# Performance work log

Measured on AMD Instinct MI355X. Metric: run time of the kernel, lower is better.

## Reference

```python
import jax, jax.numpy as jnp
import numpy as np


def setup_inputs() -> dict:
    key = jax.random.key(0)
    k1, k2 = jax.random.split(key)
    n = 12000
    dataset = jax.random.normal(k1, (n,), dtype=jnp.float32)
    weights = jax.random.uniform(k2, (n,), dtype=jnp.float32)
    return {"dataset": dataset, "weights": weights}


def reference(dataset, weights):
    # normalize weights (update_weights)
    w = weights / jnp.sum(weights)
    neff = jnp.sum(w) ** 2 / jnp.sum(w ** 2)
    # Silverman's factor (torch.std is unbiased -> ddof=1; torch.quantile is linear interp)
    std_dev = jnp.std(dataset, ddof=1)
    iqr = jnp.quantile(dataset, 0.75) - jnp.quantile(dataset, 0.25)
    sigma_hat = jnp.minimum(std_dev, iqr / 1.34)
    h = 0.9 * sigma_hat * neff ** (-0.2)
    inv_norm = 1.0 / (h * jnp.sqrt(2.0 * jnp.pi))
    # pairwise Gaussian kernel matrix: [n, n]
    diff = (dataset[:, None] - dataset[None, :]) / h
    kernel = jnp.exp(-0.5 * diff * diff) * inv_norm
    pdf = kernel @ w  # [n]
    return jnp.log(pdf + 1e-10)
```

## Files before the change

### kernel.cpp

```cpp
#include <hip/hip_runtime.h>
#include <math.h>


#define BLK 256
#define NB 2048
#define NPART 12
#define CUT 4.0f

#if defined(__has_builtin)
#if __has_builtin(__builtin_amdgcn_exp2f)
#define EXP2(x) __builtin_amdgcn_exp2f(x)
#endif
#endif
#ifndef EXP2
#define EXP2(x) exp2f(x)
#endif

__global__ __launch_bounds__(1024) void kM(const float* __restrict__ d,
                                           const float* __restrict__ w,
                                           float4* __restrict__ statP,
                                           float2* __restrict__ mmP,
                                           float* __restrict__ gZero,
                                           int n) {
    __shared__ float4 sstat[16];
    __shared__ float2 smm[16];
    const int t = threadIdx.x, lane = t & 63, wid = t >> 6;
    if (t < 512) gZero[blockIdx.x * 512 + t] = 0.f;

    const int i = blockIdx.x * 1024 + t;
    const bool ok = (i < n);
    float dv = ok ? d[i] : 0.f;
    float wv = ok ? w[i] : 0.f;
    float mn = ok ? dv : __int_as_float(0x7f800000);
    float mx = ok ? dv : __int_as_float(0xff800000);
    float s1 = wv, s2 = wv * wv, sd = dv, sd2 = dv * dv;
    for (int off = 32; off > 0; off >>= 1) {
        s1 += __shfl_down(s1, off); s2 += __shfl_down(s2, off);
        sd += __shfl_down(sd, off); sd2 += __shfl_down(sd2, off);
        mn = fminf(mn, __shfl_down(mn, off));
        mx = fmaxf(mx, __shfl_down(mx, off));
    }
    if (lane == 0) { sstat[wid] = make_float4(s1, s2, sd, sd2); smm[wid] = make_float2(mn, mx); }
    __syncthreads();
    if (t == 0) {
        float4 a = sstat[0]; float2 m = smm[0];
        for (int q = 1; q < 16; ++q) {
            float4 b = sstat[q];
            a.x += b.x; a.y += b.y; a.z += b.z; a.w += b.w;
            m.x = fminf(m.x, smm[q].x); m.y = fmaxf(m.y, smm[q].y);
        }
        statP[blockIdx.x] = a;
        mmP[blockIdx.x] = m;
    }
}

__global__ __launch_bounds__(1024) void kA(const float* __restrict__ d,
                                           const float* __restrict__ w,
                                           const float2* __restrict__ mmP,
                                           int* __restrict__ gH,
                                           float* __restrict__ gW,
                                           float* __restrict__ gWE,
                                           int n) {
    __shared__ int   hl[NB];
    __shared__ float wl[NB];
    __shared__ float wel[NB];
    const int t = threadIdx.x;

    hl[t] = 0; hl[t + 1024] = 0;
    wl[t] = 0.f; wl[t + 1024] = 0.f;
    wel[t] = 0.f; wel[t + 1024] = 0.f;

    float lo = __int_as_float(0x7f800000), hi = __int_as_float(0xff800000);
    #pragma unroll
    for (int p = 0; p < NPART; ++p) {
        float2 m = mmP[p];
        lo = fminf(lo, m.x); hi = fmaxf(hi, m.y);
    }
    const float range = hi - lo;
    const float scale = (range > 0.f) ? (float)NB / range : 0.f;
    __syncthreads();

    const int i = blockIdx.x * 1024 + t;
    if (i < n) {
        float dv = d[i], wv = w[i];
        int b = (int)((dv - lo) * scale);
        b = b < NB ? b : NB - 1;
        atomicAdd(&hl[b], 1);
        atomicAdd(&wl[b], wv);
        atomicAdd(&wel[b], wv * dv);
    }
    __syncthreads();

    #pragma unroll
    for (int k = 0; k < 2; ++k) {
        int b = t + k * 1024;
        int hv = hl[b];
        if (hv) {
            atomicAdd(&gH[b], hv);
            atomicAdd(&gW[b], wl[b]);
            atomicAdd(&gWE[b], wel[b]);
        }
    }
}

__global__ __launch_bounds__(BLK) void k3(const float* __restrict__ d,
                                          const float4* __restrict__ statP,
                                          const float2* __restrict__ mmP,
                                          const int* __restrict__ gH,
                                          const float* __restrict__ gW,
                                          const float* __restrict__ gWE,
                                          float* __restrict__ out, int n) {
    __shared__ float2 sb[NB];
    __shared__ int cum[NB];
    __shared__ int woff[4];
    __shared__ int tbin[4], tprev[4];
    __shared__ float spar[4];
    __shared__ float sred[BLK];
    const int t = threadIdx.x, lane = t & 63, wv = t >> 6;

    float lo = __int_as_float(0x7f800000), hi = __int_as_float(0xff800000);
    #pragma unroll
    for (int p = 0; p < NPART; ++p) {
        float2 m = mmP[p];
        lo = fminf(lo, m.x); hi = fmaxf(hi, m.y);
    }
    const float range = hi - lo;
    const float scale = (range > 0.f) ? (float)NB / range : 0.f;
    const float binw = (scale > 0.f) ? 1.0f / scale : 0.f;

    const int base = t * 8;
    int h8[8], pre[8];
    int s = 0;
    #pragma unroll
    for (int k = 0; k < 8; ++k) {
        int b = base + k;
        h8[k] = gH[b];
        sb[b] = make_float2(gWE[b], gW[b]);
        s += h8[k];
        pre[k] = s;
    }
    int v = s;
    for (int off = 1; off < 64; off <<= 1) {
        int u = __shfl_up(v, off);
        if (lane >= off) v += u;
    }
    if (lane == 63) woff[wv] = v;
    __syncthreads();
    int wexcl = 0;
    #pragma unroll
    for (int q = 0; q < 4; ++q) if (q < wv) wexcl += woff[q];
    const int texcl = wexcl + (v - s);
    #pragma unroll
    for (int k = 0; k < 8; ++k) cum[base + k] = texcl + pre[k];

    const double p25 = 0.25 * (double)(n - 1);
    const double p75 = 0.75 * (double)(n - 1);
    const int l25 = (int)p25, l75 = (int)p75;
    const int u25 = (l25 + 1 < n) ? l25 + 1 : l25;
    const int u75 = (l75 + 1 < n) ? l75 + 1 : l75;
    const int targets[4] = {l25, u25, l75, u75};
    #pragma unroll
    for (int k = 0; k < 8; ++k) {
        int prev = texcl + (k ? pre[k - 1] : 0);
        int incl = texcl + pre[k];
        #pragma unroll
        for (int r = 0; r < 4; ++r)
            if (prev <= targets[r] && targets[r] < incl) { tbin[r] = base + k; tprev[r] = prev; }
    }
    __syncthreads();

    if (t == 0) {
        float qv[4];
        #pragma unroll
        for (int r = 0; r < 4; ++r) {
            int b = tbin[r];
            int cnt = cum[b] - tprev[r];
            float pos = (float)b + ((float)(targets[r] - tprev[r]) + 0.5f) / (float)cnt;
            qv[r] = lo + pos * binw;
        }
        double S1 = 0, S2 = 0, Sd = 0, Sd2 = 0;
        for (int p = 0; p < NPART; ++p) {
            float4 a = statP[p];
            S1 += a.x; S2 += a.y; Sd += a.z; Sd2 += a.w;
        }
        float neff = (float)(S1 * S1 / S2);
        float varf = (float)((Sd2 - Sd * Sd / (double)n) / ((double)n - 1.0));
        float sdev = sqrtf(varf);
        float f25 = (float)(p25 - (double)l25), f75 = (float)(p75 - (double)l75);
        float q25 = qv[0] + f25 * (qv[1] - qv[0]);
        float q75 = qv[2] + f75 * (qv[3] - qv[2]);
        float sig = fminf(sdev, (q75 - q25) * (1.0f / 1.34f));
        float hb = 0.9f * sig * exp2f(-0.2f * log2f(neff));
        float rr = 0.84932180f / hb;
        float wsc = 1.0f / (hb * 2.50662827f * (float)S1);
        float delta = (scale > 0.f && rr > 0.f)
                      ? ceilf(CUT * scale / rr) + 2.0f : (float)NB;
        spar[0] = rr; spar[1] = wsc; spar[2] = delta;
    }
    __syncthreads();
    const float rr = spar[0], wsc = spar[1];
    const int delta = (int)spar[2];

    #pragma unroll
    for (int k = 0; k < 8; ++k) {
        int b = base + k;
        float2 vr = sb[b];
        float W = vr.y;
        float mu = (W > 0.f) ? (vr.x / W) : 0.f;
        sb[b] = make_float2(mu * rr, W * wsc);
    }
    __syncthreads();

    const int i = blockIdx.x * 64 + lane;
    const float di = (i < n) ? d[i] : 0.f;
    const float ei = di * rr;
    int bi = (int)((di - lo) * scale);
    bi = bi < NB ? bi : NB - 1; if (bi < 0) bi = 0;
    int b0 = bi - delta; if (b0 < 0) b0 = 0;
    int b1 = bi + delta; if (b1 > NB - 1) b1 = NB - 1;
    const int len = b1 - b0 + 1;
    const int q = (len + 3) >> 2;
    int ws_ = b0 + wv * q;
    int we_ = ws_ + q; if (we_ > b1 + 1) we_ = b1 + 1;

    float acc0 = 0.f, acc1 = 0.f;
    int b = ws_;
    for (; b + 1 < we_; b += 2) {
        float2 p0 = sb[b], p1 = sb[b + 1];
        float u0 = ei - p0.x, u1 = ei - p1.x;
        acc0 = fmaf(p0.y, EXP2(-(u0 * u0)), acc0);
        acc1 = fmaf(p1.y, EXP2(-(u1 * u1)), acc1);
    }
    if (b < we_) {
        float2 p0 = sb[b];
        float u0 = ei - p0.x;
        acc0 = fmaf(p0.y, EXP2(-(u0 * u0)), acc0);
    }

    sred[wv * 64 + lane] = acc0 + acc1;
    __syncthreads();
    if (t < 64) {
        int ii = blockIdx.x * 64 + t;
        if (ii < n) {
            float p = sred[t] + sred[64 + t] + sred[128 + t] + sred[192 + t];
            out[ii] = logf(p + 1e-10f);
        }
    }
}

extern "C" void kernel_launch(void* const* d_in, const int* in_sizes, int n_in,
                              void* d_out, int out_size, void* d_ws, size_t ws_size,
                              hipStream_t stream) {
    const float* d = (const float*)d_in[0];
    const float* w = (const float*)d_in[1];
    float* out = (float*)d_out;
    const int n = in_sizes[0];

    const int nmax = ((n + 63) / 64) * 64;
    const int G3 = nmax / 64;

    float*  wsf   = (float*)d_ws;
    float4* statP = (float4*)wsf;
    float2* mmP   = (float2*)(wsf + 48);
    float*  gZero = wsf + 80;
    int*    gH    = (int*)(wsf + 80);
    float*  gW    = wsf + 80 + NB;
    float*  gWE   = wsf + 80 + 2 * NB;

    kM<<<NPART, 1024, 0, stream>>>(d, w, statP, mmP, gZero, n);
    kA<<<NPART, 1024, 0, stream>>>(d, w, mmP, gH, gW, gWE, n);
    k3<<<G3, BLK, 0, stream>>>(d, statP, mmP, gH, gW, gWE, out, n);
}
```

Measured before the change: 24.08 us.

## Fuse stats, histogram and KDE evaluation into one redundant-per-block kernel

Replaces the three-kernel pipeline (partial stats, global histogram via atomics, evaluation) with a single kernel. Each block independently reads the whole 12000-element dataset to compute stats, min/max and a shared-memory binned histogram, then runs the evaluation for its 64 outputs. This removes two kernel launches and the global atomics and workspace traffic between them, at the cost of every one of ~188 blocks redundantly scanning all inputs twice and building its own histogram with shared-memory atomics.

```diff
diff --git a/kernel.cpp b/kernel.cpp
--- a/kernel.cpp
+++ b/kernel.cpp
@@ -4,7 +4,6 @@
 
 #define BLK 256
 #define NB 2048
-#define NPART 12
 #define CUT 4.0f
 
 #if defined(__has_builtin)
@@ -16,126 +15,65 @@
 #define EXP2(x) exp2f(x)
 #endif
 
-__global__ __launch_bounds__(1024) void kM(const float* __restrict__ d,
-                                           const float* __restrict__ w,
-                                           float4* __restrict__ statP,
-                                           float2* __restrict__ mmP,
-                                           float* __restrict__ gZero,
-                                           int n) {
-    __shared__ float4 sstat[16];
-    __shared__ float2 smm[16];
-    const int t = threadIdx.x, lane = t & 63, wid = t >> 6;
-    if (t < 512) gZero[blockIdx.x * 512 + t] = 0.f;
-
-    const int i = blockIdx.x * 1024 + t;
-    const bool ok = (i < n);
-    float dv = ok ? d[i] : 0.f;
-    float wv = ok ? w[i] : 0.f;
-    float mn = ok ? dv : __int_as_float(0x7f800000);
-    float mx = ok ? dv : __int_as_float(0xff800000);
-    float s1 = wv, s2 = wv * wv, sd = dv, sd2 = dv * dv;
+__global__ __launch_bounds__(BLK) void kde_all(const float* __restrict__ d,
+                                               const float* __restrict__ w,
+                                               float* __restrict__ out, int n) {
+    __shared__ int   hist[NB];
+    __shared__ float lW[NB];
+    __shared__ float lWE[NB];
+    __shared__ float2 sb[NB];
+    __shared__ float4 sstat[4];
+    __shared__ float2 smm[4];
+    __shared__ int woff[4];
+    __shared__ int tbin[4], tprev[4];
+    __shared__ float spar[4];
+    __shared__ float sred[BLK];
+    const int t = threadIdx.x, lane = t & 63, wv = t >> 6;
+
+    #pragma unroll
+    for (int k = 0; k < 8; ++k) {
+        int b = t + k * BLK;
+        hist[b] = 0; lW[b] = 0.f; lWE[b] = 0.f;
+    }
+
+    float s1 = 0.f, s2 = 0.f, sd = 0.f, sd2 = 0.f;
+    float mn = __int_as_float(0x7f800000), mx = __int_as_float(0xff800000);
+    for (int i = t; i < n; i += BLK) {
+        float dv = d[i], wt = w[i];
+        s1 += wt; s2 += wt * wt; sd += dv; sd2 += dv * dv;
+        mn = fminf(mn, dv); mx = fmaxf(mx, dv);
+    }
     for (int off = 32; off > 0; off >>= 1) {
         s1 += __shfl_down(s1, off); s2 += __shfl_down(s2, off);
         sd += __shfl_down(sd, off); sd2 += __shfl_down(sd2, off);
         mn = fminf(mn, __shfl_down(mn, off));
         mx = fmaxf(mx, __shfl_down(mx, off));
     }
-    if (lane == 0) { sstat[wid] = make_float4(s1, s2, sd, sd2); smm[wid] = make_float2(mn, mx); }
-    __syncthreads();
-    if (t == 0) {
-        float4 a = sstat[0]; float2 m = smm[0];
-        for (int q = 1; q < 16; ++q) {
-            float4 b = sstat[q];
-            a.x += b.x; a.y += b.y; a.z += b.z; a.w += b.w;
-            m.x = fminf(m.x, smm[q].x); m.y = fmaxf(m.y, smm[q].y);
-        }
-        statP[blockIdx.x] = a;
-        mmP[blockIdx.x] = m;
-    }
-}
-
-__global__ __launch_bounds__(1024) void kA(const float* __restrict__ d,
-                                           const float* __restrict__ w,
-                                           const float2* __restrict__ mmP,
-                                           int* __restrict__ gH,
-                                           float* __restrict__ gW,
-                                           float* __restrict__ gWE,
-                                           int n) {
-    __shared__ int   hl[NB];
-    __shared__ float wl[NB];
-    __shared__ float wel[NB];
-    const int t = threadIdx.x;
-
-    hl[t] = 0; hl[t + 1024] = 0;
-    wl[t] = 0.f; wl[t + 1024] = 0.f;
-    wel[t] = 0.f; wel[t + 1024] = 0.f;
-
-    float lo = __int_as_float(0x7f800000), hi = __int_as_float(0xff800000);
-    #pragma unroll
-    for (int p = 0; p < NPART; ++p) {
-        float2 m = mmP[p];
-        lo = fminf(lo, m.x); hi = fmaxf(hi, m.y);
-    }
-    const float range = hi - lo;
-    const float scale = (range > 0.f) ? (float)NB / range : 0.f;
-    __syncthreads();
-
-    const int i = blockIdx.x * 1024 + t;
-    if (i < n) {
-        float dv = d[i], wv = w[i];
-        int b = (int)((dv - lo) * scale);
-        b = b < NB ? b : NB - 1;
-        atomicAdd(&hl[b], 1);
-        atomicAdd(&wl[b], wv);
-        atomicAdd(&wel[b], wv * dv);
-    }
-    __syncthreads();
-
-    #pragma unroll
-    for (int k = 0; k < 2; ++k) {
-        int b = t + k * 1024;
-        int hv = hl[b];
-        if (hv) {
-            atomicAdd(&gH[b], hv);
-            atomicAdd(&gW[b], wl[b]);
-            atomicAdd(&gWE[b], wel[b]);
-        }
-    }
-}
-
-__global__ __launch_bounds__(BLK) void k3(const float* __restrict__ d,
-                                          const float4* __restrict__ statP,
-                                          const float2* __restrict__ mmP,
-                                          const int* __restrict__ gH,
-                                          const float* __restrict__ gW,
-                                          const float* __restrict__ gWE,
-                                          float* __restrict__ out, int n) {
-    __shared__ float2 sb[NB];
-    __shared__ int cum[NB];
-    __shared__ int woff[4];
-    __shared__ int tbin[4], tprev[4];
-    __shared__ float spar[4];
-    __shared__ float sred[BLK];
-    const int t = threadIdx.x, lane = t & 63, wv = t >> 6;
-
-    float lo = __int_as_float(0x7f800000), hi = __int_as_float(0xff800000);
-    #pragma unroll
-    for (int p = 0; p < NPART; ++p) {
-        float2 m = mmP[p];
-        lo = fminf(lo, m.x); hi = fmaxf(hi, m.y);
-    }
+    if (lane == 0) { sstat[wv] = make_float4(s1, s2, sd, sd2); smm[wv] = make_float2(mn, mx); }
+    __syncthreads();
+    float lo = smm[0].x, hi = smm[0].y;
+    #pragma unroll
+    for (int q = 1; q < 4; ++q) { lo = fminf(lo, smm[q].x); hi = fmaxf(hi, smm[q].y); }
     const float range = hi - lo;
     const float scale = (range > 0.f) ? (float)NB / range : 0.f;
     const float binw = (scale > 0.f) ? 1.0f / scale : 0.f;
 
+    for (int i = t; i < n; i += BLK) {
+        float dv = d[i], wt = w[i];
+        int b = (int)((dv - lo) * scale);
+        b = b < NB ? b : NB - 1;
+        atomicAdd(&hist[b], 1);
+        atomicAdd(&lW[b], wt);
+        atomicAdd(&lWE[b], wt * dv);
+    }
+    __syncthreads();
+
     const int base = t * 8;
     int h8[8], pre[8];
     int s = 0;
     #pragma unroll
     for (int k = 0; k < 8; ++k) {
-        int b = base + k;
-        h8[k] = gH[b];
-        sb[b] = make_float2(gWE[b], gW[b]);
+        h8[k] = hist[base + k];
         s += h8[k];
         pre[k] = s;
     }
@@ -151,7 +89,7 @@
     for (int q = 0; q < 4; ++q) if (q < wv) wexcl += woff[q];
     const int texcl = wexcl + (v - s);
     #pragma unroll
-    for (int k = 0; k < 8; ++k) cum[base + k] = texcl + pre[k];
+    for (int k = 0; k < 8; ++k) hist[base + k] = texcl + pre[k];
 
     const double p25 = 0.25 * (double)(n - 1);
     const double p75 = 0.75 * (double)(n - 1);
@@ -174,13 +112,14 @@
         #pragma unroll
         for (int r = 0; r < 4; ++r) {
             int b = tbin[r];
-            int cnt = cum[b] - tprev[r];
+            int cnt = hist[b] - tprev[r];
             float pos = (float)b + ((float)(targets[r] - tprev[r]) + 0.5f) / (float)cnt;
             qv[r] = lo + pos * binw;
         }
         double S1 = 0, S2 = 0, Sd = 0, Sd2 = 0;
-        for (int p = 0; p < NPART; ++p) {
-            float4 a = statP[p];
+        #pragma unroll
+        for (int q = 0; q < 4; ++q) {
+            float4 a = sstat[q];
             S1 += a.x; S2 += a.y; Sd += a.z; Sd2 += a.w;
         }
         float neff = (float)(S1 * S1 / S2);
@@ -204,9 +143,8 @@
     #pragma unroll
     for (int k = 0; k < 8; ++k) {
         int b = base + k;
-        float2 vr = sb[b];
-        float W = vr.y;
-        float mu = (W > 0.f) ? (vr.x / W) : 0.f;
+        float W = lW[b];
+        float mu = (W > 0.f) ? (lWE[b] / W) : 0.f;
         sb[b] = make_float2(mu * rr, W * wsc);
     }
     __syncthreads();
@@ -257,17 +195,7 @@
     const int n = in_sizes[0];
 
     const int nmax = ((n + 63) / 64) * 64;
-    const int G3 = nmax / 64;
-
-    float*  wsf   = (float*)d_ws;
-    float4* statP = (float4*)wsf;
-    float2* mmP   = (float2*)(wsf + 48);
-    float*  gZero = wsf + 80;
-    int*    gH    = (int*)(wsf + 80);
-    float*  gW    = wsf + 80 + NB;
-    float*  gWE   = wsf + 80 + 2 * NB;
-
-    kM<<<NPART, 1024, 0, stream>>>(d, w, statP, mmP, gZero, n);
-    kA<<<NPART, 1024, 0, stream>>>(d, w, mmP, gH, gW, gWE, n);
-    k3<<<G3, BLK, 0, stream>>>(d, statP, mmP, gH, gW, gWE, out, n);
+    const int G = nmax / 64;
+
+    kde_all<<<G, BLK, 0, stream>>>(d, w, out, n);
 }
```

Result: slower. 51.12 us (+112.3%).

## Fuse stats and histogram kernels with a flag-based inter-block barrier

Applied to the files above, without the earlier changes.

Merges the min/max/moment reduction kernel and the histogram kernel into a single launch. The 12 blocks publish their partials and then spin on per-block flags in workspace, which acts as a grid-wide barrier. The eval kernel resets the flags for the next call. The histogram now uses direct global atomics per element instead of a shared-memory histogram followed by a flush, which removes one kernel launch and gap but puts more atomic traffic on global memory. The barrier assumes all 12 blocks are co-resident, and that the zeroing writes are visible after the fence.

```diff
diff --git a/kernel.cpp b/kernel.cpp
--- a/kernel.cpp
+++ b/kernel.cpp
@@ -6,6 +6,7 @@
 #define NB 2048
 #define NPART 12
 #define CUT 4.0f
+#define MAGIC 0x13579BDF
 
 #if defined(__has_builtin)
 #if __has_builtin(__builtin_amdgcn_exp2f)
@@ -16,18 +17,23 @@
 #define EXP2(x) exp2f(x)
 #endif
 
-__global__ __launch_bounds__(1024) void kM(const float* __restrict__ d,
-                                           const float* __restrict__ w,
-                                           float4* __restrict__ statP,
-                                           float2* __restrict__ mmP,
-                                           float* __restrict__ gZero,
-                                           int n) {
+__global__ __launch_bounds__(1024) void prep_k(const float* __restrict__ d,
+                                               const float* __restrict__ w,
+                                               float4* __restrict__ statP,
+                                               float2* __restrict__ mmP,
+                                               int* __restrict__ flagA,
+                                               float* __restrict__ gZero,
+                                               int* __restrict__ gH,
+                                               float* __restrict__ gW,
+                                               float* __restrict__ gWE,
+                                               int n) {
     __shared__ float4 sstat[16];
     __shared__ float2 smm[16];
-    const int t = threadIdx.x, lane = t & 63, wid = t >> 6;
-    if (t < 512) gZero[blockIdx.x * 512 + t] = 0.f;
-
-    const int i = blockIdx.x * 1024 + t;
+    const int t = threadIdx.x, lane = t & 63, wid = t >> 6, blk = blockIdx.x;
+
+    if (t < 512) gZero[blk * 512 + t] = 0.f;
+
+    const int i = blk * 1024 + t;
     const bool ok = (i < n);
     float dv = ok ? d[i] : 0.f;
     float wv = ok ? w[i] : 0.f;
@@ -49,26 +55,17 @@
             a.x += b.x; a.y += b.y; a.z += b.z; a.w += b.w;
             m.x = fminf(m.x, smm[q].x); m.y = fmaxf(m.y, smm[q].y);
         }
-        statP[blockIdx.x] = a;
-        mmP[blockIdx.x] = m;
-    }
-}
-
-__global__ __launch_bounds__(1024) void kA(const float* __restrict__ d,
-                                           const float* __restrict__ w,
-                                           const float2* __restrict__ mmP,
-                                           int* __restrict__ gH,
-                                           float* __restrict__ gW,
-                                           float* __restrict__ gWE,
-                                           int n) {
-    __shared__ int   hl[NB];
-    __shared__ float wl[NB];
-    __shared__ float wel[NB];
-    const int t = threadIdx.x;
-
-    hl[t] = 0; hl[t + 1024] = 0;
-    wl[t] = 0.f; wl[t + 1024] = 0.f;
-    wel[t] = 0.f; wel[t + 1024] = 0.f;
+        statP[blk] = a;
+        mmP[blk] = m;
+        __threadfence();
+        atomicExch(&flagA[blk], MAGIC);
+        for (int j = 0; j < NPART; ++j) {
+            while (atomicCAS(&flagA[j], MAGIC, MAGIC) != MAGIC)
+                __builtin_amdgcn_s_sleep(16);
+        }
+    }
+    __syncthreads();
+    __threadfence();
 
     float lo = __int_as_float(0x7f800000), hi = __int_as_float(0xff800000);
     #pragma unroll
@@ -78,38 +75,24 @@
     }
     const float range = hi - lo;
     const float scale = (range > 0.f) ? (float)NB / range : 0.f;
-    __syncthreads();
-
-    const int i = blockIdx.x * 1024 + t;
-    if (i < n) {
-        float dv = d[i], wv = w[i];
+
+    if (ok) {
         int b = (int)((dv - lo) * scale);
         b = b < NB ? b : NB - 1;
-        atomicAdd(&hl[b], 1);
-        atomicAdd(&wl[b], wv);
-        atomicAdd(&wel[b], wv * dv);
-    }
-    __syncthreads();
-
-    #pragma unroll
-    for (int k = 0; k < 2; ++k) {
-        int b = t + k * 1024;
-        int hv = hl[b];
-        if (hv) {
-            atomicAdd(&gH[b], hv);
-            atomicAdd(&gW[b], wl[b]);
-            atomicAdd(&gWE[b], wel[b]);
-        }
+        atomicAdd(&gH[b], 1);
+        atomicAdd(&gW[b], wv);
+        atomicAdd(&gWE[b], wv * dv);
     }
 }
 
-__global__ __launch_bounds__(BLK) void k3(const float* __restrict__ d,
-                                          const float4* __restrict__ statP,
-                                          const float2* __restrict__ mmP,
-                                          const int* __restrict__ gH,
-                                          const float* __restrict__ gW,
-                                          const float* __restrict__ gWE,
-                                          float* __restrict__ out, int n) {
+__global__ __launch_bounds__(BLK) void eval_k(const float* __restrict__ d,
+                                              const float4* __restrict__ statP,
+                                              const float2* __restrict__ mmP,
+                                              int* __restrict__ flagA,
+                                              const int* __restrict__ gH,
+                                              const float* __restrict__ gW,
+                                              const float* __restrict__ gWE,
+                                              float* __restrict__ out, int n) {
     __shared__ float2 sb[NB];
     __shared__ int cum[NB];
     __shared__ int woff[4];
@@ -117,6 +100,8 @@
     __shared__ float spar[4];
     __shared__ float sred[BLK];
     const int t = threadIdx.x, lane = t & 63, wv = t >> 6;
+
+    if (blockIdx.x == 0 && t < NPART) flagA[t] = 0;
 
     float lo = __int_as_float(0x7f800000), hi = __int_as_float(0xff800000);
     #pragma unroll
@@ -179,6 +164,7 @@
             qv[r] = lo + pos * binw;
         }
         double S1 = 0, S2 = 0, Sd = 0, Sd2 = 0;
+        #pragma unroll
         for (int p = 0; p < NPART; ++p) {
             float4 a = statP[p];
             S1 += a.x; S2 += a.y; Sd += a.z; Sd2 += a.w;
@@ -257,17 +243,17 @@
     const int n = in_sizes[0];
 
     const int nmax = ((n + 63) / 64) * 64;
-    const int G3 = nmax / 64;
+    const int G = nmax / 64;
 
     float*  wsf   = (float*)d_ws;
     float4* statP = (float4*)wsf;
     float2* mmP   = (float2*)(wsf + 48);
-    float*  gZero = wsf + 80;
-    int*    gH    = (int*)(wsf + 80);
-    float*  gW    = wsf + 80 + NB;
-    float*  gWE   = wsf + 80 + 2 * NB;
-
-    kM<<<NPART, 1024, 0, stream>>>(d, w, statP, mmP, gZero, n);
-    kA<<<NPART, 1024, 0, stream>>>(d, w, mmP, gH, gW, gWE, n);
-    k3<<<G3, BLK, 0, stream>>>(d, statP, mmP, gH, gW, gWE, out, n);
+    int*    flagA = (int*)(wsf + 72);
+    float*  gZero = wsf + 88;
+    int*    gH    = (int*)(wsf + 88);
+    float*  gW    = wsf + 88 + NB;
+    float*  gWE   = wsf + 88 + 2 * NB;
+
+    prep_k<<<NPART, 1024, 0, stream>>>(d, w, statP, mmP, flagA, gZero, gH, gW, gWE, n);
+    eval_k<<<G, BLK, 0, stream>>>(d, statP, mmP, flagA, gH, gW, gWE, out, n);
 }
```

After: 30.79 us. +27.9%, slower.
